# Kernel tuning notes

Hardware: AMD Instinct MI355X
Metric: run time of the kernel (lower is better)

Reference implementation:

```python
import jax, jax.numpy as jnp
import numpy as np

STRIDE = 16
PRE_K = 600
POST_K = 100
NMS_T = 0.7


def _gen_anchors(base=16.0, ratios=(0.5, 1.0, 2.0), scales=(8.0, 16.0, 32.0)):
    a = []
    for s in scales:
        for r in ratios:
            w = base * s * (r ** 0.5)
            h = base * s / (r ** 0.5)
            a.append([-w / 2, -h / 2, w / 2, h / 2])
    return jnp.asarray(a, jnp.float32)  # [9,4]


def _conv(x, w, b, pad):
    y = jax.lax.conv_general_dilated(x, w, (1, 1), [(pad, pad), (pad, pad)],
                                     dimension_numbers=("NCHW", "OIHW", "NCHW"))
    return y + b[None, :, None, None]


def _decode(deltas, anchors):
    w = anchors[:, 2] - anchors[:, 0]
    h = anchors[:, 3] - anchors[:, 1]
    cx = anchors[:, 0] + 0.5 * w
    cy = anchors[:, 1] + 0.5 * h
    dx, dy, dw, dh = deltas[:, 0], deltas[:, 1], deltas[:, 2], deltas[:, 3]
    pcx = cx + dx * w
    pcy = cy + dy * h
    pw = w * jnp.exp(dw)
    ph = h * jnp.exp(dh)
    return jnp.stack([pcx - 0.5 * pw, pcy - 0.5 * ph,
                      pcx + 0.5 * pw, pcy + 0.5 * ph], axis=-1)


def _nms_keep(boxes, thresh):
    # boxes already sorted by score descending; returns bool keep mask [N]
    x1, y1, x2, y2 = boxes[:, 0], boxes[:, 1], boxes[:, 2], boxes[:, 3]
    area = (x2 - x1) * (y2 - y1)
    xx1 = jnp.maximum(x1[:, None], x1[None, :])
    yy1 = jnp.maximum(y1[:, None], y1[None, :])
    xx2 = jnp.minimum(x2[:, None], x2[None, :])
    yy2 = jnp.minimum(y2[:, None], y2[None, :])
    inter = jnp.maximum(xx2 - xx1, 0.0) * jnp.maximum(yy2 - yy1, 0.0)
    iou = inter / (area[:, None] + area[None, :] - inter)
    n = boxes.shape[0]
    idx = jnp.arange(n)

    def body(i, keep):
        suppress = keep[i] & (iou[i] > thresh) & (idx > i)
        return keep & ~suppress

    return jax.lax.fori_loop(0, n, body, jnp.ones((n,), bool))


def setup_inputs() -> dict:
    key = jax.random.key(0)
    ks = jax.random.split(key, 7)
    C_in, C_mid, A = 256, 256, 9
    feats = jax.random.normal(ks[0], (4, C_in, 128, 128), jnp.float32)
    conv_w = jax.random.normal(ks[1], (C_mid, C_in, 3, 3), jnp.float32) * 0.02
    conv_b = jnp.zeros((C_mid,), jnp.float32)
    cls_w = jax.random.normal(ks[2], (A, C_mid, 1, 1), jnp.float32) * 0.05
    cls_b = jnp.zeros((A,), jnp.float32)
    bbox_w = jax.random.normal(ks[3], (A * 4, C_mid, 1, 1), jnp.float32) * 0.02
    bbox_b = jnp.zeros((A * 4,), jnp.float32)
    return {"features": feats, "conv_w": conv_w, "conv_b": conv_b,
            "cls_w": cls_w, "cls_b": cls_b, "bbox_w": bbox_w, "bbox_b": bbox_b,
            "image_h": 2048, "image_w": 2048}


def reference(features, conv_w, conv_b, cls_w, cls_b, bbox_w, bbox_b, image_h, image_w):
    B, _, H, W = features.shape
    A = cls_w.shape[0]
    t = jax.nn.relu(_conv(features, conv_w, conv_b, 1))
    logits = _conv(t, cls_w, cls_b, 0)        # [B,A,H,W]
    bbox_deltas = _conv(t, bbox_w, bbox_b, 0)  # [B,4A,H,W]

    anchors = _gen_anchors()
    sx = jnp.arange(W, dtype=jnp.float32) * STRIDE
    sy = jnp.arange(H, dtype=jnp.float32) * STRIDE
    gy, gx = jnp.meshgrid(sy, sx, indexing="ij")
    shifts = jnp.stack([gx, gy, gx, gy], axis=2).reshape(-1, 4)  # [HW,4]
    anchors_all = (anchors[None, :, :] + shifts[:, None, :]).reshape(-1, 4)  # [HW*A,4]

    scores = jnp.transpose(logits, (0, 2, 3, 1)).reshape(B, -1)          # [B,HWA]
    deltas = jnp.transpose(bbox_deltas, (0, 2, 3, 1)).reshape(B, -1, 4)  # [B,HWA,4]

    img_w = jnp.float32(image_w)
    img_h = jnp.float32(image_h)

    def per_image(s, d):
        p = _decode(d, anchors_all)
        p = jnp.stack([jnp.clip(p[:, 0], 0.0, img_w),
                       jnp.clip(p[:, 1], 0.0, img_h),
                       jnp.clip(p[:, 2], 0.0, img_w),
                       jnp.clip(p[:, 3], 0.0, img_h)], axis=-1)
        _, topi = jax.lax.top_k(s, PRE_K)
        p = p[topi]                                # [PRE_K,4] sorted by score
        keep = _nms_keep(p, NMS_T)
        order = jnp.argsort(jnp.where(keep, 0, 1), stable=True)  # kept first, score order
        sel = order[:POST_K]
        valid = keep[sel]
        return p[sel] * valid[:, None].astype(p.dtype)  # zero-pad suppressed slots

    return jax.vmap(per_image)(scores, deltas)  # [B,POST_K,4]
```

## Files before the change

### kernel.cpp

```cpp
#include <hip/hip_runtime.h>
#include <cstdint>
#include <cstddef>

#define BB 4
#define CIN 256
#define HH 128
#define WW 128
#define NANCH (HH*WW*9)
#define PRE_K 600
#define POST_K 100
#define NMS_T 0.7f
#define CAND_CAP 8192
#define CCNT_STRIDE 16

typedef _Float16 f16x8 __attribute__((ext_vector_type(8)));
typedef float    f32x4 __attribute__((ext_vector_type(4)));

#define WS_SCORES 0
#define WS_DELTAS (BB*NANCH)
#define WS_WHI    (WS_DELTAS + BB*NANCH*4)
#define WS_WLO    (WS_WHI + 9*256*128)
#define WS_HIST   (WS_WLO + 9*256*128)
#define WS_CCNT   (WS_HIST + 8192)
#define WS_CAND   (WS_CCNT + 64)
#define WS_PHI    (WS_CAND + BB*CAND_CAP*2)
#define WS_PLANE_F 8388608
#define WS_PLO    (WS_PHI + WS_PLANE_F)
#define WS_ZERO   (WS_PLO + WS_PLANE_F)
#define WS_TOTAL_FULL (WS_ZERO + 16)
#define WS_TOTAL_MIN  WS_PHI

__device__ inline unsigned score_key(float f) {
    unsigned u = __float_as_uint(f);
    return (u & 0x80000000u) ? ~u : (u | 0x80000000u);
}

__device__ inline void decode_box(unsigned idx, const float* __restrict__ deltas,
                                  int b, float fw, float fh, float* o4)
{
    const int a   = (int)(idx % 9u);
    const int n4  = (int)(idx / 9u);
    const int hh_ = n4 >> 7;
    const int ww_ = n4 & 127;
    const int si_ = a / 3, ri = a % 3;
    const double sq = (ri == 0) ? 0.70710678118654752440 : ((ri == 1) ? 1.0 : 1.41421356237309504880);
    const double sc = (si_ == 0) ? 8.0 : ((si_ == 1) ? 16.0 : 32.0);
    const float half_w = (float)(16.0 * sc * sq * 0.5);
    const float half_h = (float)(16.0 * sc / sq * 0.5);
    const float shx = 16.f * (float)ww_;
    const float shy = 16.f * (float)hh_;
    const float x1a = shx - half_w, x2a = shx + half_w;
    const float y1a = shy - half_h, y2a = shy + half_h;
    const float aw = x2a - x1a, ah = y2a - y1a;
    const float acx = x1a + 0.5f*aw, acy = y1a + 0.5f*ah;
    const float* d = deltas + ((size_t)b*NANCH + idx) * 4;
    const float dx = d[0], dy = d[1], dw = d[2], dh = d[3];
    const float pcx = acx + dx*aw;
    const float pcy = acy + dy*ah;
    const float pw  = aw * expf(dw);
    const float ph  = ah * expf(dh);
    o4[0] = fminf(fmaxf(pcx - 0.5f*pw, 0.f), fw);
    o4[1] = fminf(fmaxf(pcy - 0.5f*ph, 0.f), fh);
    o4[2] = fminf(fmaxf(pcx + 0.5f*pw, 0.f), fw);
    o4[3] = fminf(fmaxf(pcy + 0.5f*ph, 0.f), fh);
}

__global__ __launch_bounds__(256)
void prep_all(const float* __restrict__ feat, const float* __restrict__ convw,
              _Float16* __restrict__ pHi, _Float16* __restrict__ pLo,
              _Float16* __restrict__ whi, _Float16* __restrict__ wlo,
              float* __restrict__ zeroPg, unsigned* __restrict__ ghist,
              int prepBlocks)
{
    const int blk = blockIdx.x;
    if (blk < prepBlocks) {
        const int id = blk * 256 + threadIdx.x;
        if (blk == 0 && threadIdx.x < 16) zeroPg[threadIdx.x] = 0.f;
        const int gx = id & 127;
        const int gy = (id >> 7) & 127;
        const int ck = (id >> 14) & 7;
        const int b  = id >> 17;
        const int g  = (((gx + 1) >> 1) & 1) | (((gy + 1) & 1) << 1);
        const float* fb = feat + ((size_t)(b*256 + ck*32) << 14) + (gy << 7) + gx;
        f16x8 gh[4], gl[4];
        #pragma unroll
        for (int icg = 0; icg < 4; ++icg)
            #pragma unroll
            for (int k = 0; k < 8; ++k) {
                const float v = fb[(size_t)(icg*8 + k) << 14] * 16.f;
                const _Float16 h = (_Float16)v;
                gh[icg][k] = h;
                gl[icg][k] = (_Float16)(v - (float)h);
            }
        char* Hc = (char*)pHi + (size_t)id * 64;
        char* Lc = (char*)pLo + (size_t)id * 64;
        #pragma unroll
        for (int icg = 0; icg < 4; ++icg) {
            const int p = icg ^ g;
            *(f16x8*)(Hc + p*16) = gh[icg];
            *(f16x8*)(Lc + p*16) = gl[icg];
        }
    } else if (blk < prepBlocks + 256) {
        const int g = (blk - prepBlocks) * 256 + threadIdx.x;
        if (g >= 65536) return;
        const int oc = g >> 8, ic = g & 255;
        const int chunk = ic >> 5, icl = ic & 31;
        #pragma unroll
        for (int t = 0; t < 9; ++t) {
            const float v = convw[(size_t)g*9 + t] * 64.f;
            const _Float16 h = (_Float16)v;
            const _Float16 lo = (_Float16)(v - (float)h);
            const size_t o = (size_t)((t*8 + chunk)*256 + oc)*32 + icl;
            whi[o] = h;
            wlo[o] = lo;
        }
    } else {
        const int id = (blk - prepBlocks - 256) * 256 + threadIdx.x;
        if (id < 8256) ghist[id] = 0u;
    }
}

__global__ __launch_bounds__(512, 2)
void conv_mfma(const float* __restrict__ feat, const float* __restrict__ convb,
               const _Float16* __restrict__ whi, const _Float16* __restrict__ wlo,
               const float* __restrict__ clsw, const float* __restrict__ bboxw,
               const float* __restrict__ clsb, const float* __restrict__ bboxb,
               const _Float16* __restrict__ pHi, const _Float16* __restrict__ pLo,
               const float* __restrict__ zeroPg, unsigned* __restrict__ ghist,
               float* __restrict__ scores, float* __restrict__ deltas)
{
    __shared__ __align__(16) unsigned char smem[87040];
    float* sBias = (float*)(smem + 86016);

    const int bid = blockIdx.x;
    const int b  = bid >> 6;
    const int ty = (bid >> 3) & 7;
    const int tx = bid & 7;
    const int h0 = ty*16, c0 = tx*16;
    const int tid = threadIdx.x;
    const int w   = tid >> 6;
    const int wm  = w >> 1;
    const int wph = w & 1;
    const int l  = tid & 63;
    const int q  = l >> 4;
    const int c  = l & 15;

    const float* featb = feat + (size_t)b*CIN*HH*WW;
    const int wOff = (wm*64 + c)*32 + q*8;

    if (tid < 256) sBias[tid] = convb[tid] * 1024.f;

    int sdesc[3];
    #pragma unroll
    for (int it = 0; it < 3; ++it) {
        const int e = it*512 + tid;
        if (e < 1344) {
            const int Yl = e / 72, rem = e - Yl*72;
            const int Xl = rem >> 2, p = rem & 3;
            const int gy = h0 - 1 + Yl, gx = c0 - 1 + Xl;
            sdesc[it] = (((unsigned)gy < 128u) && ((unsigned)gx < 128u))
                        ? ((((gy << 7) + gx) << 6) + (p << 4)) : -1;
        } else sdesc[it] = -2;
    }

    auto stage = [&](int ck, int buf) {
        unsigned char* hb = smem + buf*21504;
        unsigned char* lb = smem + 43008 + buf*21504;
        if (pHi) {
            const size_t pb = ((size_t)(b*8 + ck)) << 20;
            #pragma unroll
            for (int pl = 0; pl < 2; ++pl) {
                const char* Ps = (const char*)(pl ? pLo : pHi) + pb;
                unsigned char* Pd = pl ? lb : hb;
                #pragma unroll
                for (int it = 0; it < 3; ++it) {
                    if (sdesc[it] != -2) {
                        const char* src = (sdesc[it] >= 0) ? Ps + sdesc[it]
                                                           : (const char*)zeroPg;
                        __builtin_amdgcn_global_load_lds(
                            (const __attribute__((address_space(1))) void*)src,
                            (__attribute__((address_space(3))) void*)(Pd + it*8192 + tid*16),
                            16, 0, 0);
                    }
                }
            }
        } else {
            const int ic0s = ck*32;
            for (int e = tid; e < 1296; e += 512) {
                const int icg = e / 324, s = e - icg*324;
                const int Y = s / 18, X = s - Y*18;
                const int gy = h0 - 1 + Y, gx = c0 - 1 + X;
                const int g = ((X >> 1) & 1) | ((Y & 1) << 1);
                const bool inb = ((unsigned)gy < 128u) && ((unsigned)gx < 128u);
                f16x8 hv, lv;
                #pragma unroll
                for (int k = 0; k < 8; ++k) {
                    float v = 0.f;
                    if (inb) v = featb[((size_t)(ic0s + icg*8 + k)*HH + gy)*WW + gx];
                    v *= 16.f;
                    const _Float16 h = (_Float16)v;
                    hv[k] = h;
                    lv[k] = (_Float16)(v - (float)h);
                }
                const int base = s*64 + ((icg ^ g) << 4);
                *(f16x8*)(hb + base) = hv;
                *(f16x8*)(lb + base) = lv;
            }
        }
    };

    stage(0, 0);
    __syncthreads();

    f32x4 acc[4][8];
    #pragma unroll
    for (int mf = 0; mf < 4; ++mf) {
        const f32x4 bv = *(const f32x4*)(sBias + (wm*64 + mf*16 + 4*q));
        #pragma unroll
        for (int nf = 0; nf < 8; ++nf) acc[mf][nf] = bv;
    }

    for (int chunk = 0; chunk < 8; ++chunk) {
        const int cur = chunk & 1;
        if (chunk + 1 < 8) stage(chunk + 1, cur ^ 1);
        const unsigned char* hb = smem + cur*21504;
        const unsigned char* lb = smem + 43008 + cur*21504;

        #pragma unroll 3
        for (int t = 0; t < 9; ++t) {
            const int ky = t / 3, kx = t - ky*3;
            const _Float16* pWh = whi + (size_t)(t*8 + chunk)*8192 + wOff;
            const _Float16* pWl = wlo + (size_t)(t*8 + chunk)*8192 + wOff;
            f16x8 ah[4], al[4];
            #pragma unroll
            for (int mf = 0; mf < 4; ++mf) {
                ah[mf] = *(const f16x8*)(const void*)(pWh + mf*512);
                al[mf] = *(const f16x8*)(const void*)(pWl + mf*512);
            }
            #pragma unroll
            for (int nfh = 0; nfh < 2; ++nfh) {
                f16x8 bh[4], bl[4];
                #pragma unroll
                for (int j = 0; j < 4; ++j) {
                    const int nf = nfh*4 + j;
                    const int Y = wph*8 + (nf >> 1)*2 + (c >> 3) + ky;
                    const int X = (nf & 1)*8 + (c & 7) + kx;
                    const int g = ((X >> 1) & 1) | ((Y & 1) << 1);
                    const int addr = (Y*18 + X)*64 + ((q ^ g) << 4);
                    bh[j] = *(const f16x8*)(hb + addr);
                    bl[j] = *(const f16x8*)(lb + addr);
                }
                #pragma unroll
                for (int mf = 0; mf < 4; ++mf)
                    #pragma unroll
                    for (int j = 0; j < 4; ++j) {
                        acc[mf][nfh*4+j] = __builtin_amdgcn_mfma_f32_16x16x32_f16(ah[mf], bh[j], acc[mf][nfh*4+j], 0, 0, 0);
                        acc[mf][nfh*4+j] = __builtin_amdgcn_mfma_f32_16x16x32_f16(ah[mf], bl[j], acc[mf][nfh*4+j], 0, 0, 0);
                        acc[mf][nfh*4+j] = __builtin_amdgcn_mfma_f32_16x16x32_f16(al[mf], bh[j], acc[mf][nfh*4+j], 0, 0, 0);
                    }
            }
        }
        __syncthreads();
    }

    #pragma unroll
    for (int mf = 0; mf < 4; ++mf)
        #pragma unroll
        for (int nf = 0; nf < 8; ++nf)
            #pragma unroll
            for (int r = 0; r < 4; ++r)
                acc[mf][nf][r] = fmaxf(acc[mf][nf][r], 0.f) * 0.0009765625f;

    float*    sW15  = (float*)smem;
    float*    sPart = (float*)(smem + 15360);
    unsigned* sHist = (unsigned*)(smem + 76800);

    for (int e = tid; e < 2048; e += 512) sHist[e] = 0u;

    for (int g = 0; g < 3; ++g) {
        __syncthreads();
        for (int e = tid; e < 3840; e += 512) {
            const int chl = e >> 8, o = e & 255;
            const int ch = g*15 + chl;
            sW15[e] = (ch < 9) ? clsw[ch*256 + o] : bboxw[(ch - 9)*256 + o];
        }
        __syncthreads();
        for (int chl = 0; chl < 15; ++chl) {
            f32x4 wv[4];
            #pragma unroll
            for (int mf = 0; mf < 4; ++mf)
                wv[mf] = *(const f32x4*)(sW15 + chl*256 + wm*64 + mf*16 + 4*q);
            float p[8];
            #pragma unroll
            for (int nf = 0; nf < 8; ++nf) {
                float s = 0.f;
                #pragma unroll
                for (int mf = 0; mf < 4; ++mf)
                    #pragma unroll
                    for (int r = 0; r < 4; ++r)
                        s += wv[mf][r] * acc[mf][nf][r];
                s += __shfl_xor(s, 16, 64);
                s += __shfl_xor(s, 32, 64);
                p[nf] = s;
            }
            const float v0 = (q == 0) ? p[0] : (q == 1) ? p[1] : (q == 2) ? p[2] : p[3];
            const float v1 = (q == 0) ? p[4] : (q == 1) ? p[5] : (q == 2) ? p[6] : p[7];
            sPart[(w*15 + chl)*128 + q*16 + c]      = v0;
            sPart[(w*15 + chl)*128 + 64 + q*16 + c] = v1;
        }
        __syncthreads();
        for (int e = tid; e < 3840; e += 512) {
            const int chl = e >> 8, pxg = e & 255;
            const int ph = pxg >> 7, pxl = pxg & 127;
            float s = 0.f;
            #pragma unroll
            for (int wmq = 0; wmq < 4; ++wmq)
                s += sPart[((wmq*2 + ph)*15 + chl)*128 + pxl];
            const int ch = g*15 + chl;
            s += (ch < 9) ? clsb[ch] : bboxb[ch - 9];
            const int nf = pxl >> 4, cc2 = pxl & 15;
            const int Y = ph*8 + (nf >> 1)*2 + (cc2 >> 3);
            const int X = (nf & 1)*8 + (cc2 & 7);
            const int gy = h0 + Y, gx = c0 + X;
            const int n4 = gy*WW + gx;
            if (ch < 9) {
                scores[(size_t)b*NANCH + n4*9 + ch] = s;
                atomicAdd(&sHist[score_key(s) >> 21], 1u);
            } else {
                const int cc = ch - 9;
                deltas[((size_t)b*NANCH + n4*9 + (cc >> 2))*4 + (cc & 3)] = s;
            }
        }
    }
    for (int e = tid; e < 2048; e += 512) {
        const unsigned cv = sHist[e];
        if (cv) atomicAdd(&ghist[b*2048 + e], cv);
    }
}

__device__ inline void find_thresh(const unsigned* hist, int NB, unsigned target, unsigned* shv)
{
    const int tid = threadIdx.x;
    if (tid < 64) {
        const int gsz = NB >> 5;
        unsigned gsum = 0;
        if (tid < 32)
            for (int k = 0; k < gsz; ++k)
                gsum += hist[tid*gsz + ((k + tid) & (gsz-1))];
        unsigned suf = gsum;
        #pragma unroll
        for (int d = 1; d < 32; d <<= 1) {
            const unsigned t = __shfl_down(suf, d, 64);
            if (tid + d < 32) suf += t;
        }
        const unsigned long long m = __ballot(tid < 32 && suf >= target);
        const int G = 63 - __clzll(m);
        unsigned caboveG = 0;
        { const unsigned t = __shfl(suf, G+1, 64); if (G < 31) caboveG = t; }
        unsigned h = 0;
        if (tid < gsz) h = hist[G*gsz + tid];
        unsigned wsuf = h;
        #pragma unroll
        for (int d = 1; d < 64; d <<= 1) {
            const unsigned t = __shfl_down(wsuf, d, 64);
            if (tid + d < gsz) wsuf += t;
        }
        const unsigned long long m2 = __ballot(tid < gsz && (caboveG + wsuf) >= target);
        const int L = 63 - __clzll(m2);
        if (tid == L) { shv[0] = (unsigned)(G*gsz + L); shv[1] = caboveG + wsuf - h; }
    }
}

__global__ __launch_bounds__(256)
void filter_kernel(const float* __restrict__ scores, const unsigned* __restrict__ ghist,
                   unsigned* __restrict__ ccnt, unsigned long long* __restrict__ cand)
{
    __shared__ unsigned h[2048];
    __shared__ unsigned shv[8];
    __shared__ unsigned long long lbuf[2304];
    __shared__ unsigned lcnt, gbase;
    const int blk = blockIdx.x;
    const int b = blk >> 6, s = blk & 63;
    const int tid = threadIdx.x;
    const unsigned* hb = ghist + b*2048;
    if (tid == 0) lcnt = 0u;
    for (int e = tid; e < 2048; e += 256) h[e] = hb[e];
    __syncthreads();
    find_thresh(h, 2048, PRE_K, shv);
    __syncthreads();
    const unsigned T1 = shv[0];
    const unsigned C  = shv[1] + h[T1];
    const float* si = scores + (size_t)b*NANCH + s*2304;
    if (C <= (unsigned)CAND_CAP) {
        #pragma unroll
        for (int k = 0; k < 9; ++k) {
            const int i = tid + k*256;
            const unsigned u = score_key(si[i]);
            if ((u >> 21) >= T1) {
                const unsigned p = atomicAdd(&lcnt, 1u);
                lbuf[p] = ((unsigned long long)(~u) << 32) | (unsigned)(s*2304 + i);
            }
        }
        __syncthreads();
        if (tid == 0) gbase = atomicAdd(&ccnt[b*CCNT_STRIDE], lcnt);
        __syncthreads();
        const unsigned nL = lcnt, base = gbase;
        for (unsigned e = tid; e < nL; e += 256)
            cand[(size_t)b*CAND_CAP + base + e] = lbuf[e];
    } else if (s == 0 && tid == 0) {
        ccnt[b*CCNT_STRIDE] = 0x7FFFFFFFu;
    }
}

__device__ inline unsigned long long shfl_u64(unsigned long long v, int src) {
    const int lo = __shfl((int)(v & 0xffffffffull), src, 64);
    const int hi = __shfl((int)(v >> 32), src, 64);
    return ((unsigned long long)(unsigned)hi << 32) | (unsigned)lo;
}

__global__ __launch_bounds__(1024)
void post_kernel(const float* __restrict__ scores, const float* __restrict__ deltas,
                 const unsigned* __restrict__ ccnt, const unsigned long long* __restrict__ cand,
                 const int* __restrict__ imh, const int* __restrict__ imw,
                 float* __restrict__ out)
{
    __shared__ unsigned long long cnd[CAND_CAP];
    __shared__ float bx[PRE_K][4];
    __shared__ unsigned long long mrow[PRE_K][10];
    __shared__ unsigned hist[2048];
    __shared__ unsigned long long arr[1024];
    __shared__ unsigned tiebuf[1024];
    __shared__ unsigned shv[8];
    __shared__ unsigned long long keepw[10];
    __shared__ unsigned wpfx[11];
    __shared__ int sel[POST_K];
    const int b = blockIdx.x, tid = threadIdx.x;
    const float* si = scores + (size_t)b*NANCH;
    const float fw = (float)imw[0], fh = (float)imh[0];

    const unsigned n = ccnt[b*CCNT_STRIDE];
    const bool fast = (n <= (unsigned)CAND_CAP);

    if (fast) {
        for (int e = tid; e < (int)n; e += 1024)
            cnd[e] = cand[(size_t)b*CAND_CAP + e];
        __syncthreads();
        for (int e = tid; e < (int)n; e += 1024) {
            const unsigned long long cv = cnd[e];
            unsigned rank = 0;
            for (int e2 = 0; e2 < (int)n; ++e2)
                rank += (cnd[e2] < cv) ? 1u : 0u;
            if (rank < PRE_K) {
                float o4[4];
                decode_box((unsigned)cv, deltas, b, fw, fh, o4);
                bx[rank][0] = o4[0]; bx[rank][1] = o4[1];
                bx[rank][2] = o4[2]; bx[rank][3] = o4[3];
            }
        }
        __syncthreads();
    } else {
        for (int i = tid; i < 2048; i += 1024) hist[i] = 0;
        __syncthreads();
        for (int i = tid; i < NANCH; i += 1024)
            atomicAdd(&hist[score_key(si[i]) >> 21], 1u);
        __syncthreads();
        find_thresh(hist, 2048, PRE_K, shv);
        __syncthreads();
        const unsigned T1 = shv[0], gtA = shv[1];
        __syncthreads();

        for (int i = tid; i < 2048; i += 1024) hist[i] = 0;
        __syncthreads();
        for (int i = tid; i < NANCH; i += 1024) {
            const unsigned u = score_key(si[i]);
            if ((u >> 21) == T1) atomicAdd(&hist[(u >> 10) & 0x7FFu], 1u);
        }
        __syncthreads();
        find_thresh(hist, 2048, PRE_K - gtA, shv);
        __syncthreads();
        const unsigned T2 = shv[0], gtB = shv[1];
        const unsigned top22 = (T1 << 11) | T2;
        __syncthreads();

        for (int i = tid; i < 1024; i += 1024) hist[i] = 0;
        __syncthreads();
        for (int i = tid; i < NANCH; i += 1024) {
            const unsigned u = score_key(si[i]);
            if ((u >> 10) == top22) atomicAdd(&hist[u & 0x3FFu], 1u);
        }
        __syncthreads();
        find_thresh(hist, 1024, PRE_K - gtA - gtB, shv);
        if (tid == 0) { shv[4] = 0; shv[5] = 0; }
        __syncthreads();
        const unsigned u_thr = (top22 << 10) | shv[0];
        const unsigned n_greater = gtA + gtB + shv[1];
        __syncthreads();

        for (int i = tid; i < NANCH; i += 1024) {
            const unsigned u = score_key(si[i]);
            if (u > u_thr) {
                const unsigned p = atomicAdd(&shv[4], 1u);
                arr[p] = ((unsigned long long)(~u) << 32) | (unsigned)i;
            } else if (u == u_thr) {
                const unsigned p = atomicAdd(&shv[5], 1u);
                if (p < 1024u) tiebuf[p] = (unsigned)i;
            }
        }
        __syncthreads();
        const unsigned cnt_tie = (shv[5] > 1024u) ? 1024u : shv[5];
        if ((unsigned)tid >= cnt_tie) tiebuf[tid] = 0xFFFFFFFFu;

        for (unsigned k = 2; k <= 1024; k <<= 1)
            for (unsigned j = k >> 1; j > 0; j >>= 1) {
                __syncthreads();
                const unsigned i = (unsigned)tid, ixj = i ^ j;
                if (ixj > i) {
                    const unsigned a = tiebuf[i], cc = tiebuf[ixj];
                    if ((a > cc) == ((i & k) == 0)) { tiebuf[i] = cc; tiebuf[ixj] = a; }
                }
            }
        __syncthreads();
        const unsigned ties_needed = PRE_K - n_greater;
        if ((unsigned)tid < ties_needed)
            arr[n_greater + tid] = ((unsigned long long)(~u_thr) << 32) | tiebuf[tid];
        if (tid >= PRE_K) arr[tid] = ~0ull;

        for (unsigned k = 2; k <= 1024; k <<= 1)
            for (unsigned j = k >> 1; j > 0; j >>= 1) {
                __syncthreads();
                const unsigned i = (unsigned)tid, ixj = i ^ j;
                if (ixj > i) {
                    const unsigned long long a = arr[i], cc = arr[ixj];
                    if ((a > cc) == ((i & k) == 0)) { arr[i] = cc; arr[ixj] = a; }
                }
            }
        __syncthreads();

        if (tid < PRE_K) {
            float o4[4];
            decode_box((unsigned)arr[tid], deltas, b, fw, fh, o4);
            bx[tid][0] = o4[0]; bx[tid][1] = o4[1]; bx[tid][2] = o4[2]; bx[tid][3] = o4[3];
        }
        __syncthreads();
    }

    for (int item = tid; item < PRE_K*10; item += 1024) {
        const int i  = item / 10;
        const int wj = item - i*10;
        unsigned long long m = 0ull;
        const int jbase = wj * 64;
        if (jbase + 63 > i) {
            const float xi1 = bx[i][0], yi1 = bx[i][1], xi2 = bx[i][2], yi2 = bx[i][3];
            const float ai = (xi2 - xi1) * (yi2 - yi1);
            for (int bit = 0; bit < 64; ++bit) {
                const int j = jbase + bit;
                if (j < PRE_K && j > i) {
                    const float xx1 = fmaxf(xi1, bx[j][0]);
                    const float yy1 = fmaxf(yi1, bx[j][1]);
                    const float xx2 = fminf(xi2, bx[j][2]);
                    const float yy2 = fminf(yi2, bx[j][3]);
                    const float inter = fmaxf(xx2 - xx1, 0.f) * fmaxf(yy2 - yy1, 0.f);
                    const float aj = (bx[j][2] - bx[j][0]) * (bx[j][3] - bx[j][1]);
                    const float iou = inter / (ai + aj - inter);
                    if (iou > NMS_T) m |= (1ull << bit);
                }
            }
        }
        mrow[i][wj] = m;
    }
    __syncthreads();

    if (tid < 64) {
        const int lane = tid;
        unsigned long long kwv;
        if (lane < 9)       kwv = ~0ull;
        else if (lane == 9) kwv = (1ull << (PRE_K - 576)) - 1;
        else                kwv = 0ull;
        for (int w = 0; w < 10; ++w) {
            const int base = w*64;
            const int nb = (w == 9) ? (PRE_K - 576) : 64;
            if (lane == w) {
                for (int bit = 0; bit < nb; ++bit) {
                    const unsigned long long mm = mrow[base + bit][w];
                    if ((kwv >> bit) & 1ull) kwv &= ~mm;
                }
            }
            const unsigned long long fw2 = shfl_u64(kwv, w);
            if (lane > w && lane < 10) {
                for (int bit = 0; bit < nb; ++bit) {
                    const unsigned long long mm = mrow[base + bit][lane];
                    if ((fw2 >> bit) & 1ull) kwv &= ~mm;
                }
            }
        }
        if (lane < 10) keepw[lane] = kwv;
    }
    __syncthreads();
    if (tid == 0) {
        unsigned ccount = 0;
        #pragma unroll
        for (int w = 0; w < 10; ++w) { wpfx[w] = ccount; ccount += (unsigned)__popcll(keepw[w]); }
        wpfx[10] = ccount;
    }
    if (tid < POST_K) sel[tid] = -1;
    __syncthreads();
    if (tid < PRE_K) {
        const int w = tid >> 6, bit = tid & 63;
        const unsigned long long kw = keepw[w];
        if ((kw >> bit) & 1ull) {
            const unsigned rank = wpfx[w] + (unsigned)__popcll(kw & ((1ull << bit) - 1ull));
            if (rank < POST_K) sel[rank] = tid;
        }
    }
    __syncthreads();
    if (tid < POST_K) {
        const int s_ = sel[tid];
        float o0 = 0.f, o1 = 0.f, o2 = 0.f, o3 = 0.f;
        if (s_ >= 0) { o0 = bx[s_][0]; o1 = bx[s_][1]; o2 = bx[s_][2]; o3 = bx[s_][3]; }
        float* o = out + (size_t)b*POST_K*4 + tid*4;
        o[0] = o0; o[1] = o1; o[2] = o2; o[3] = o3;
    }
}

extern "C" void kernel_launch(void* const* d_in, const int* in_sizes, int n_in,
                              void* d_out, int out_size, void* d_ws, size_t ws_size,
                              hipStream_t stream) {
    const float* feat  = (const float*)d_in[0];
    const float* convw = (const float*)d_in[1];
    const float* convb = (const float*)d_in[2];
    const float* clsw  = (const float*)d_in[3];
    const float* clsb  = (const float*)d_in[4];
    const float* bboxw = (const float*)d_in[5];
    const float* bboxb = (const float*)d_in[6];
    const int*   imh   = (const int*)d_in[7];
    const int*   imw   = (const int*)d_in[8];

    if (ws_size < (size_t)WS_TOTAL_MIN * sizeof(float)) return;
    const bool use_prep = ws_size >= (size_t)WS_TOTAL_FULL * sizeof(float);

    float*    scores = (float*)d_ws + WS_SCORES;
    float*    deltas = (float*)d_ws + WS_DELTAS;
    _Float16* whi    = (_Float16*)((float*)d_ws + WS_WHI);
    _Float16* wlo    = (_Float16*)((float*)d_ws + WS_WLO);
    unsigned* ghist  = (unsigned*)((float*)d_ws + WS_HIST);
    unsigned* ccnt   = (unsigned*)((float*)d_ws + WS_CCNT);
    unsigned long long* cand = (unsigned long long*)((float*)d_ws + WS_CAND);
    _Float16* pHi    = use_prep ? (_Float16*)((float*)d_ws + WS_PHI) : nullptr;
    _Float16* pLo    = use_prep ? (_Float16*)((float*)d_ws + WS_PLO) : nullptr;
    float*    zeroPg = use_prep ? ((float*)d_ws + WS_ZERO) : nullptr;
    float*    outp   = (float*)d_out;

    const int prepBlocks = use_prep ? 2048 : 0;
    prep_all<<<dim3(prepBlocks + 256 + 33), dim3(256), 0, stream>>>(
        feat, convw, pHi, pLo, whi, wlo, zeroPg, ghist, prepBlocks);
    conv_mfma<<<dim3(256), dim3(512), 0, stream>>>(feat, convb, whi, wlo, clsw, bboxw,
                                                   clsb, bboxb, pHi, pLo, zeroPg, ghist,
                                                   scores, deltas);
    filter_kernel<<<dim3(256), dim3(256), 0, stream>>>(scores, ghist, ccnt, cand);
    post_kernel<<<dim3(BB), dim3(1024), 0, stream>>>(scores, deltas, ccnt, cand,
                                                     imh, imw, outp);
}
```

Before: 426.9 us.

## Split candidate ranking into separate multi-block kernel before NMS

Moves the O(n^2) rank-by-counting of top-k candidates out of the 4-block post kernel into a new 128-block rank_kernel. Each block ranks 256 candidates and writes the decoded top-600 boxes to a workspace buffer, which post_kernel then loads. This spreads the quadratic ranking across many CUs instead of four, and frees the large candidate shared-memory array in post_kernel. The cost is an extra kernel launch and a global round trip for the boxes. The workspace layout also grows, shifting the plane buffers, which raises the minimum workspace size needed for the prep path.

```diff
diff --git a/kernel.cpp b/kernel.cpp
--- a/kernel.cpp
+++ b/kernel.cpp
@@ -23,7 +23,8 @@
 #define WS_HIST   (WS_WLO + 9*256*128)
 #define WS_CCNT   (WS_HIST + 8192)
 #define WS_CAND   (WS_CCNT + 64)
-#define WS_PHI    (WS_CAND + BB*CAND_CAP*2)
+#define WS_BOX6   (WS_CAND + BB*CAND_CAP*2)
+#define WS_PHI    (WS_BOX6 + BB*PRE_K*4)
 #define WS_PLANE_F 8388608
 #define WS_PLO    (WS_PHI + WS_PLANE_F)
 #define WS_ZERO   (WS_PLO + WS_PLANE_F)
@@ -412,6 +413,37 @@
     }
 }
 
+__global__ __launch_bounds__(256)
+void rank_kernel(const unsigned* __restrict__ ccnt, const unsigned long long* __restrict__ cand,
+                 const float* __restrict__ deltas,
+                 const int* __restrict__ imh, const int* __restrict__ imw,
+                 float* __restrict__ boxes6)
+{
+    __shared__ unsigned long long cnd[CAND_CAP];
+    const int blk = blockIdx.x;
+    const int b = blk >> 5, s = blk & 31;
+    const int tid = threadIdx.x;
+    const unsigned n = ccnt[b*CCNT_STRIDE];
+    if (n > (unsigned)CAND_CAP) return;
+    const int e0 = s*256;
+    if ((unsigned)e0 >= n) return;
+    for (int e = tid; e < (int)n; e += 256)
+        cnd[e] = cand[(size_t)b*CAND_CAP + e];
+    __syncthreads();
+    const int e = e0 + tid;
+    if (e >= (int)n) return;
+    const unsigned long long cv = cnd[e];
+    unsigned rank = 0;
+    for (int e2 = 0; e2 < (int)n; ++e2)
+        rank += (cnd[e2] < cv) ? 1u : 0u;
+    if (rank < PRE_K) {
+        float o4[4];
+        decode_box((unsigned)cv, deltas, b, (float)imw[0], (float)imh[0], o4);
+        float* o = boxes6 + ((size_t)b*PRE_K + rank)*4;
+        o[0] = o4[0]; o[1] = o4[1]; o[2] = o4[2]; o[3] = o4[3];
+    }
+}
+
 __device__ inline unsigned long long shfl_u64(unsigned long long v, int src) {
     const int lo = __shfl((int)(v & 0xffffffffull), src, 64);
     const int hi = __shfl((int)(v >> 32), src, 64);
@@ -420,11 +452,10 @@
 
 __global__ __launch_bounds__(1024)
 void post_kernel(const float* __restrict__ scores, const float* __restrict__ deltas,
-                 const unsigned* __restrict__ ccnt, const unsigned long long* __restrict__ cand,
+                 const unsigned* __restrict__ ccnt, const float* __restrict__ boxes6,
                  const int* __restrict__ imh, const int* __restrict__ imw,
                  float* __restrict__ out)
 {
-    __shared__ unsigned long long cnd[CAND_CAP];
     __shared__ float bx[PRE_K][4];
     __shared__ unsigned long long mrow[PRE_K][10];
     __shared__ unsigned hist[2048];
@@ -442,21 +473,8 @@
     const bool fast = (n <= (unsigned)CAND_CAP);
 
     if (fast) {
-        for (int e = tid; e < (int)n; e += 1024)
-            cnd[e] = cand[(size_t)b*CAND_CAP + e];
-        __syncthreads();
-        for (int e = tid; e < (int)n; e += 1024) {
-            const unsigned long long cv = cnd[e];
-            unsigned rank = 0;
-            for (int e2 = 0; e2 < (int)n; ++e2)
-                rank += (cnd[e2] < cv) ? 1u : 0u;
-            if (rank < PRE_K) {
-                float o4[4];
-                decode_box((unsigned)cv, deltas, b, fw, fh, o4);
-                bx[rank][0] = o4[0]; bx[rank][1] = o4[1];
-                bx[rank][2] = o4[2]; bx[rank][3] = o4[3];
-            }
-        }
+        for (int e = tid; e < PRE_K*4; e += 1024)
+            bx[e >> 2][e & 3] = boxes6[(size_t)b*PRE_K*4 + e];
         __syncthreads();
     } else {
         for (int i = tid; i < 2048; i += 1024) hist[i] = 0;
@@ -645,6 +663,7 @@
     unsigned* ghist  = (unsigned*)((float*)d_ws + WS_HIST);
     unsigned* ccnt   = (unsigned*)((float*)d_ws + WS_CCNT);
     unsigned long long* cand = (unsigned long long*)((float*)d_ws + WS_CAND);
+    float*    boxes6 = (float*)d_ws + WS_BOX6;
     _Float16* pHi    = use_prep ? (_Float16*)((float*)d_ws + WS_PHI) : nullptr;
     _Float16* pLo    = use_prep ? (_Float16*)((float*)d_ws + WS_PLO) : nullptr;
     float*    zeroPg = use_prep ? ((float*)d_ws + WS_ZERO) : nullptr;
@@ -657,6 +676,7 @@
                                                    clsb, bboxb, pHi, pLo, zeroPg, ghist,
                                                    scores, deltas);
     filter_kernel<<<dim3(256), dim3(256), 0, stream>>>(scores, ghist, ccnt, cand);
-    post_kernel<<<dim3(BB), dim3(1024), 0, stream>>>(scores, deltas, ccnt, cand,
+    rank_kernel<<<dim3(128), dim3(256), 0, stream>>>(ccnt, cand, deltas, imh, imw, boxes6);
+    post_kernel<<<dim3(BB), dim3(1024), 0, stream>>>(scores, deltas, ccnt, boxes6,
                                                      imh, imw, outp);
 }
```

Result: faster. 406.0 us (-4.9%).
